# Kernel tuning notes

Hardware: AMD Instinct MI355X
Metric: run time of the kernel (lower is better)

The kernel has to match this reference:

```python
import jax, jax.numpy as jnp
import numpy as np

N_HEADS = 32
N_KV_HEADS = 8
HEAD_DIM = 128
EPS = 1e-6


def _rope_tables(seq_len, dim, base=10000.0):
    inv_freq = 1.0 / (base ** (np.arange(0, dim, 2, dtype=np.float32) / dim))
    t = np.arange(seq_len, dtype=np.float32)
    freqs = np.outer(t, inv_freq)            # [S, d/2]
    emb = np.concatenate([freqs, freqs], -1)  # [S, d]
    return jnp.asarray(np.cos(emb)), jnp.asarray(np.sin(emb))


def setup_inputs() -> dict:
    key = jax.random.key(0)
    ks = jax.random.split(key, 6)
    B, S, H = 1, 2048, 4096
    d = HEAD_DIM
    cos, sin = _rope_tables(S, d)
    return {
        "hidden_states": jax.random.normal(ks[0], (B, S, H), jnp.float32),
        "position_ids": jnp.broadcast_to(jnp.arange(S, dtype=jnp.int64 if jax.config.jax_enable_x64 else jnp.int32), (B, S)),
        "Wq": jax.random.normal(ks[1], (N_HEADS * d, H), jnp.float32) * 0.02,
        "Wk": jax.random.normal(ks[2], (N_KV_HEADS * d, H), jnp.float32) * 0.02,
        "Wv": jax.random.normal(ks[3], (N_KV_HEADS * d, H), jnp.float32) * 0.02,
        "Wo": jax.random.normal(ks[4], (H, N_HEADS * d), jnp.float32) * 0.02,
        "q_norm_w": jnp.ones((d,), jnp.float32),
        "k_norm_w": jnp.ones((d,), jnp.float32),
        "cos": cos,
        "sin": sin,
    }


def _rmsnorm(x, w):
    xf = x.astype(jnp.float32)
    var = jnp.mean(xf * xf, axis=-1, keepdims=True)
    return (w * (xf * jax.lax.rsqrt(var + EPS))).astype(x.dtype)


def _rotate_half(x):
    x1, x2 = jnp.split(x, 2, axis=-1)
    return jnp.concatenate([-x2, x1], axis=-1)


def reference(hidden_states, position_ids, Wq, Wk, Wv, Wo, q_norm_w, k_norm_w, cos, sin):
    B, S, H = hidden_states.shape
    d = HEAD_DIM
    n_rep = N_HEADS // N_KV_HEADS

    # projections -> [B, nH, S, d] / [B, nKV, S, d]
    q = (hidden_states @ Wq.T).reshape(B, S, N_HEADS, d).transpose(0, 2, 1, 3)
    k = (hidden_states @ Wk.T).reshape(B, S, N_KV_HEADS, d).transpose(0, 2, 1, 3)
    v = (hidden_states @ Wv.T).reshape(B, S, N_KV_HEADS, d).transpose(0, 2, 1, 3)

    # per-head QK RMSNorm
    q = _rmsnorm(q, q_norm_w)
    k = _rmsnorm(k, k_norm_w)

    # RoPE: cos/sin gathered by position_ids -> [B, 1, S, d]
    c = cos[position_ids][:, None, :, :]
    s = sin[position_ids][:, None, :, :]
    q = q * c + _rotate_half(q) * s
    k = k * c + _rotate_half(k) * s

    # GQA: repeat kv heads
    k = jnp.repeat(k, n_rep, axis=1)
    v = jnp.repeat(v, n_rep, axis=1)

    # causal SDPA
    scale = 1.0 / jnp.sqrt(jnp.asarray(d, jnp.float32))
    scores = jnp.einsum("bhqd,bhkd->bhqk", q, k) * scale
    causal = jnp.tril(jnp.ones((S, S), bool))
    scores = jnp.where(causal[None, None], scores, jnp.finfo(scores.dtype).min)
    probs = jax.nn.softmax(scores, axis=-1)
    attn = jnp.einsum("bhqk,bhkd->bhqd", probs, v)

    out = attn.transpose(0, 2, 1, 3).reshape(B, S, N_HEADS * d)
    return out @ Wo.T
```

## Files before the change

### kernel.cpp

```cpp
#include <hip/hip_runtime.h>


typedef __attribute__((ext_vector_type(4))) float    f32x4;
typedef __attribute__((ext_vector_type(8))) _Float16 f16x8;
typedef __attribute__((ext_vector_type(4))) _Float16 f16x4;
typedef __attribute__((ext_vector_type(2))) _Float16 f16x2;

#define AS1 __attribute__((address_space(1)))
#define AS3 __attribute__((address_space(3)))

static __device__ __forceinline__ void gld_lds16(const void* g, void* l) {
  __builtin_amdgcn_global_load_lds((AS1 void*)(g), (AS3 void*)(l), 16, 0, 0);
}

static __device__ __forceinline__ void barrier_raw() {
  asm volatile("s_barrier" ::: "memory");
}
#define WAIT_VMCNT(n) asm volatile("s_waitcnt vmcnt(" #n ")" ::: "memory")

__global__ void f32_to_f16(const float* __restrict__ src,
                           _Float16* __restrict__ dst, int n4) {
  int i = blockIdx.x * blockDim.x + threadIdx.x;
  if (i >= n4) return;
  float4 v = ((const float4*)src)[i];
  f16x4 o = {(_Float16)v.x, (_Float16)v.y, (_Float16)v.z, (_Float16)v.w};
  ((f16x4*)dst)[i] = o;
}

__global__ void cvt4(const float* __restrict__ s0, const float* __restrict__ s1,
                     const float* __restrict__ s2, const float* __restrict__ s3,
                     _Float16* __restrict__ d0, _Float16* __restrict__ d1,
                     _Float16* __restrict__ d2, _Float16* __restrict__ d3,
                     int n0, int n1, int n2, int n3) {
  int i = blockIdx.x * blockDim.x + threadIdx.x;
  const float* s;
  _Float16* d;
  int j = i;
  if (j < n0) {
    s = s0; d = d0;
  } else if ((j -= n0) < n1) {
    s = s1; d = d1;
  } else if ((j -= n1) < n2) {
    s = s2; d = d2;
  } else if ((j -= n2) < n3) {
    s = s3; d = d3;
  } else {
    return;
  }
  float4 v = ((const float4*)s)[j];
  f16x4 o = {(_Float16)v.x, (_Float16)v.y, (_Float16)v.z, (_Float16)v.w};
  ((f16x4*)d)[j] = o;
}

template <int BN, typename CT>
__global__ __launch_bounds__(512, 2) void gemm256(
    const _Float16* __restrict__ A, const _Float16* __restrict__ B,
    CT* __restrict__ C, int N, int K) {
  constexpr int NI = BN / 64;
  constexpr int NB = NI / 2;
  __shared__ _Float16 lA[2][256 * 64];
  __shared__ _Float16 lB[2][BN * 64];
  const int tid = threadIdx.x;
  const int lane = tid & 63;
  const int wid = tid >> 6;
  const int quad = lane >> 4, l16 = lane & 15;
  const int wr = wid >> 2, wc = wid & 3;
  const int bid = blockIdx.x;
  const int m0 = (bid & 7) * 256;
  const int n0 = (bid >> 3) * BN;

  const int sr = tid >> 3, sch = tid & 7;
  const int swz = l16 & 7;

  f32x4 acc[8][NI];
#pragma unroll
  for (int i = 0; i < 8; i++)
#pragma unroll
    for (int j = 0; j < NI; j++) acc[i][j] = f32x4{0.f, 0.f, 0.f, 0.f};

  const int nt = K >> 6;

  auto stageA = [&](int bb, int h, int kt) {
#pragma unroll
    for (int u = 0; u < 2; ++u) {
      int rl = u * 64 + sr;
      int r = h * 128 + rl;
      int cg = sch ^ (rl & 7);
      gld_lds16(A + (size_t)(m0 + r) * K + kt * 64 + cg * 8,
                &lA[bb][(size_t)r * 64 + sch * 8]);
    }
  };
  auto stageB = [&](int bb, int h, int kt) {
#pragma unroll
    for (int u = 0; u < 2; ++u) {
      int rl = u * 64 + sr;
      int r = h * 128 + rl;
      int cg = sch ^ (rl & 7);
      gld_lds16(B + (size_t)(n0 + r) * K + kt * 64 + cg * 8,
                &lB[bb][(size_t)r * 64 + sch * 8]);
    }
  };

  auto ldA = [&](f16x8* dst, int qm, int bb) {
#pragma unroll
    for (int mi = 0; mi < 4; ++mi)
#pragma unroll
      for (int kk = 0; kk < 2; ++kk) {
        int row = wr * 128 + (qm * 4 + mi) * 16 + l16;
        int ch = (kk * 4 + quad) ^ swz;
        dst[mi * 2 + kk] = *(const f16x8*)&lA[bb][(size_t)row * 64 + ch * 8];
      }
  };
  auto ldB = [&](f16x8* dst, int qn, int bb) {
#pragma unroll
    for (int ni = 0; ni < NB; ++ni)
#pragma unroll
      for (int kk = 0; kk < 2; ++kk) {
        int row = wc * (BN / 4) + (qn * NB + ni) * 16 + l16;
        int ch = (kk * 4 + quad) ^ swz;
        dst[ni * 2 + kk] = *(const f16x8*)&lB[bb][(size_t)row * 64 + ch * 8];
      }
  };
  auto mmQ = [&](const f16x8* af, const f16x8* bf, int qm, int qn) {
    __builtin_amdgcn_s_setprio(1);
    __builtin_amdgcn_sched_barrier(0);
#pragma unroll
    for (int mi = 0; mi < 4; ++mi)
#pragma unroll
      for (int ni = 0; ni < NB; ++ni)
#pragma unroll
        for (int kk = 0; kk < 2; ++kk)
          acc[qm * 4 + mi][qn * NB + ni] =
              __builtin_amdgcn_mfma_f32_16x16x32_f16(
                  af[mi * 2 + kk], bf[ni * 2 + kk],
                  acc[qm * 4 + mi][qn * NB + ni], 0, 0, 0);
    __builtin_amdgcn_sched_barrier(0);
    __builtin_amdgcn_s_setprio(0);
  };

  stageA(0, 0, 0);
  stageA(0, 1, 0);
  stageB(0, 0, 0);
  if constexpr (BN == 256) stageB(0, 1, 0);
  stageB(1, 0, 1);
  if constexpr (BN == 256) stageB(1, 1, 1);
  if constexpr (BN == 256) {
    WAIT_VMCNT(4);
  } else {
    WAIT_VMCNT(2);
  }
  barrier_raw();

  f16x8 af[8], b0[2 * NB], b1[2 * NB];
  for (int t = 0; t < nt; ++t) {
    const int b = t & 1;
    const int tn1 = (t + 1 < nt) ? t + 1 : t;
    const int tn2 = (t + 2 < nt) ? t + 2 : t;
    ldA(af, 0, b);
    ldB(b0, 0, b);
    stageA(b ^ 1, 0, tn1);
    barrier_raw();
    mmQ(af, b0, 0, 0);
    barrier_raw();
    ldB(b1, 1, b);
    stageA(b ^ 1, 1, tn1);
    barrier_raw();
    mmQ(af, b1, 0, 1);
    barrier_raw();
    ldA(af, 1, b);
    stageB(b, 0, tn2);
    barrier_raw();
    mmQ(af, b1, 1, 1);
    barrier_raw();
    if constexpr (BN == 256) stageB(b, 1, tn2);
    if constexpr (BN == 256) {
      WAIT_VMCNT(4);
    } else {
      WAIT_VMCNT(2);
    }
    barrier_raw();
    mmQ(af, b0, 1, 0);
    barrier_raw();
  }

#pragma unroll
  for (int mi8 = 0; mi8 < 8; ++mi8) {
    int m = m0 + wr * 128 + mi8 * 16 + quad * 4;
#pragma unroll
    for (int ni = 0; ni < NI; ++ni) {
      int n = n0 + wc * (BN / 4) + ni * 16 + l16;
      CT* cp = C + (size_t)m * N + n;
#pragma unroll
      for (int r = 0; r < 4; ++r) cp[(size_t)r * N] = (CT)acc[mi8][ni][r];
    }
  }
}

__global__ void norm_rope(const _Float16* __restrict__ raw, int row_stride,
                          int col_off, const float* __restrict__ w,
                          const float* __restrict__ cosb,
                          const float* __restrict__ sinb,
                          const int* __restrict__ pos,
                          _Float16* __restrict__ out, int nh_log2, int S) {
  int gt = blockIdx.x * blockDim.x + threadIdx.x;
  int wid = gt >> 6, lane = gt & 63;
  int h = wid & ((1 << nh_log2) - 1);
  int s = wid >> nh_log2;
  const _Float16* x = raw + (size_t)s * row_stride + col_off + h * 128;
  f16x2 v2 = *(const f16x2*)&x[lane * 2];
  float vx = (float)v2.x, vy = (float)v2.y;
  float ss = vx * vx + vy * vy;
#pragma unroll
  for (int m = 1; m < 64; m <<= 1) ss += __shfl_xor(ss, m);
  float inv = rsqrtf(ss * (1.f / 128.f) + 1e-6f);
  int p = pos[s];
  float n0 = vx * inv * w[lane * 2];
  float n1 = vy * inv * w[lane * 2 + 1];
  float p0 = __shfl_xor(n0, 32);
  float p1 = __shfl_xor(n1, 32);
  float r0 = (lane < 32) ? -p0 : p0;
  float r1 = (lane < 32) ? -p1 : p1;
  float c0 = cosb[p * 128 + lane * 2], c1 = cosb[p * 128 + lane * 2 + 1];
  float s0 = sinb[p * 128 + lane * 2], s1 = sinb[p * 128 + lane * 2 + 1];
  f16x2 o;
  o.x = (_Float16)(n0 * c0 + r0 * s0);
  o.y = (_Float16)(n1 * c1 + r1 * s1);
  *(f16x2*)&out[((size_t)h * S + s) * 128 + lane * 2] = o;
}

__global__ __launch_bounds__(256) void v_trans(const _Float16* __restrict__ vraw,
                                               int row_stride,
                                               _Float16* __restrict__ vt,
                                               int S) {
  __shared__ _Float16 tile[64][72];
  int s0 = blockIdx.x * 64, c0 = blockIdx.y * 64;
  int t = threadIdx.x;
  int r = t >> 2, cq = (t & 3) * 16;
  const _Float16* src = vraw + (size_t)(s0 + r) * row_stride + c0 + cq;
  f16x8 u0 = *(const f16x8*)&src[0];
  f16x8 u1 = *(const f16x8*)&src[8];
#pragma unroll
  for (int j = 0; j < 8; j++) {
    tile[r][cq + j] = u0[j];
    tile[r][cq + 8 + j] = u1[j];
  }
  __syncthreads();
  int orow = t >> 2, sq = (t & 3) * 16;
  _Float16* dst = vt + (size_t)(c0 + orow) * S + s0 + sq;
  f16x8 a, b;
#pragma unroll
  for (int j = 0; j < 8; j++) a[j] = tile[sq + j][orow];
#pragma unroll
  for (int j = 0; j < 8; j++) b[j] = tile[sq + 8 + j][orow];
  *(f16x8*)&dst[0] = a;
  *(f16x8*)&dst[8] = b;
}

__global__ __launch_bounds__(256, 2) void flash_attn(
    const _Float16* __restrict__ Qh, const _Float16* __restrict__ Kh,
    const _Float16* __restrict__ Vt, _Float16* __restrict__ Oout, int S) {
  __shared__ _Float16 lK[3][32 * 128];
  __shared__ _Float16 lV[3][128 * 32];
  __shared__ _Float16 plds[4][16][40];
  const int wave = threadIdx.x >> 6, lane = threadIdx.x & 63;
  const int quad = lane >> 4, l16 = lane & 15;

  const int flat = blockIdx.y * gridDim.x + blockIdx.x;
  const int head = (flat & 7) * 4 + ((flat >> 3) & 3);
  const int px   = flat >> 5;
  const int kvh  = head >> 2;
  const _Float16* K = Kh + (size_t)kvh * S * 128;
  const _Float16* V = Vt + (size_t)kvh * 128 * S;

  const int ksw = l16 & 7;
  const int vchunk = quad ^ ((l16 >> 1) & 3);
  const float scale = 0.08838834764831845f;
  const float Mc = 5.0f;

  auto stage = [&](int kt, int bi) {
#pragma unroll
    for (int u = 0; u < 2; ++u) {
      int j = wave * 2 + u;
      int rK = j * 4 + (lane >> 4);
      int cK = (lane & 15) ^ (rK & 7);
      gld_lds16(K + (size_t)(kt * 32 + rK) * 128 + cK * 8, &lK[bi][j * 512]);
      int rV = j * 16 + (lane >> 2);
      int cV = (lane & 3) ^ ((rV >> 1) & 3);
      gld_lds16(V + (size_t)rV * S + kt * 32 + cV * 8, &lV[bi][j * 512]);
    }
  };

#pragma unroll
  for (int seg = 0; seg < 2; ++seg) {
    const int tile = seg ? (31 - px) : px;
    const int q0 = tile * 64;
    const int wq = q0 + wave * 16;
    const _Float16* Q = Qh + ((size_t)head * S + wq) * 128;

    f16x8 qf[4];
#pragma unroll
    for (int kq = 0; kq < 4; kq++)
      qf[kq] = *(const f16x8*)&Q[(size_t)l16 * 128 + kq * 32 + quad * 8];

    f32x4 o[8];
#pragma unroll
    for (int t = 0; t < 8; t++) o[t] = f32x4{0.f, 0.f, 0.f, 0.f};
    float l_i = 0.f;
    const int q_row = wq + l16;
    const int ktend = 2 * tile + 1;

    stage(0, 0);
    stage(1, 1);
    WAIT_VMCNT(4);
    barrier_raw();

    for (int kt = 0; kt <= ktend; ++kt) {
      const int cur = kt % 3;
      const bool more = (kt + 2 <= ktend);
      if (more) stage(kt + 2, (kt + 2) % 3);
      if (kt * 32 <= wq + 15) {
        f32x4 sc[2];
        sc[0] = f32x4{0.f, 0.f, 0.f, 0.f};
        sc[1] = f32x4{0.f, 0.f, 0.f, 0.f};
#pragma unroll
        for (int mt = 0; mt < 2; mt++)
#pragma unroll
          for (int kq = 0; kq < 4; kq++) {
            f16x8 kf = *(const f16x8*)&lK[cur][(mt * 16 + l16) * 128 +
                                              (((kq * 4 + quad) ^ ksw) * 8)];
            sc[mt] = __builtin_amdgcn_mfma_f32_16x16x32_f16(kf, qf[kq], sc[mt],
                                                            0, 0, 0);
          }
        float p[2][4];
        float rsum = 0.f;
#pragma unroll
        for (int mt = 0; mt < 2; mt++)
#pragma unroll
          for (int r = 0; r < 4; r++) {
            int kcol = kt * 32 + mt * 16 + quad * 4 + r;
            float e = __expf(fmaf(sc[mt][r], scale, -Mc));
            e = (kcol <= q_row) ? e : 0.f;
            p[mt][r] = e;
            rsum += e;
          }
        rsum += __shfl_xor(rsum, 16);
        rsum += __shfl_xor(rsum, 32);
        l_i += rsum;
        f16x4 pk0 = {(_Float16)p[0][0], (_Float16)p[0][1], (_Float16)p[0][2],
                     (_Float16)p[0][3]};
        f16x4 pk1 = {(_Float16)p[1][0], (_Float16)p[1][1], (_Float16)p[1][2],
                     (_Float16)p[1][3]};
        *(f16x4*)&plds[wave][l16][quad * 4] = pk0;
        *(f16x4*)&plds[wave][l16][16 + quad * 4] = pk1;
        f16x8 pf = *(const f16x8*)&plds[wave][l16][quad * 8];
#pragma unroll
        for (int t = 0; t < 8; t++) {
          f16x8 vf = *(const f16x8*)&lV[cur][(t * 16 + l16) * 32 + vchunk * 8];
          o[t] = __builtin_amdgcn_mfma_f32_16x16x32_f16(vf, pf, o[t], 0, 0, 0);
        }
      }
      if (more) {
        WAIT_VMCNT(4);
      } else {
        WAIT_VMCNT(0);
      }
      barrier_raw();
    }

    const float invl = 1.f / l_i;
    _Float16* op = Oout + (size_t)q_row * 4096 + head * 128 + quad * 4;
#pragma unroll
    for (int t = 0; t < 8; t++) {
      f16x4 ov = {(_Float16)(o[t][0] * invl), (_Float16)(o[t][1] * invl),
                  (_Float16)(o[t][2] * invl), (_Float16)(o[t][3] * invl)};
      *(f16x4*)&op[t * 16] = ov;
    }
  }
}

extern "C" void kernel_launch(void* const* d_in, const int* in_sizes, int n_in,
                              void* d_out, int out_size, void* d_ws,
                              size_t ws_size, hipStream_t stream) {
  const int S = 2048, H = 4096, NH = 32, NKV = 8, D = 128;
  const int NQKV = NH * D + 2 * NKV * D;
  const float* hs   = (const float*)d_in[0];
  const int*   pos  = (const int*)d_in[1];
  const float* Wq   = (const float*)d_in[2];
  const float* Wk   = (const float*)d_in[3];
  const float* Wv   = (const float*)d_in[4];
  const float* Wo   = (const float*)d_in[5];
  const float* qw   = (const float*)d_in[6];
  const float* kw   = (const float*)d_in[7];
  const float* cosb = (const float*)d_in[8];
  const float* sinb = (const float*)d_in[9];
  float* out = (float*)d_out;

  char* ws = (char*)d_ws;
  _Float16* wqkv    = (_Float16*)(ws + 0);
  _Float16* hid_bf  = (_Float16*)(ws + 50331648);
  _Float16* qkv_f16 = (_Float16*)(ws + 67108864);
  _Float16* q_bf    = (_Float16*)(ws + 117440512);
  _Float16* k_bf    = (_Float16*)(ws + 134217728);
  _Float16* v_t     = (_Float16*)(ws + 138412032);
  _Float16* attn_bf = (_Float16*)(ws + 96468992);
  _Float16* wo_bf   = (_Float16*)(ws + 0);

  const int n_hs4 = S * H / 4;
  const int n_wq4 = NH * D * H / 4;
  const int n_wk4 = NKV * D * H / 4;
  const int n_wv4 = NKV * D * H / 4;
  const int ncvt = n_hs4 + n_wq4 + n_wk4 + n_wv4;
  cvt4<<<(ncvt + 255) / 256, 256, 0, stream>>>(
      hs, Wq, Wk, Wv, hid_bf, wqkv, wqkv + (size_t)H * H,
      wqkv + (size_t)(H + NKV * D) * H, n_hs4, n_wq4, n_wk4, n_wv4);

  gemm256<256, _Float16><<<dim3((NQKV / 256) * 8), 512, 0, stream>>>(
      hid_bf, wqkv, qkv_f16, NQKV, H);
  f32_to_f16<<<(H * H / 4 + 255) / 256, 256, 0, stream>>>(Wo, wo_bf, H * H / 4);

  norm_rope<<<S * NH / 4, 256, 0, stream>>>(qkv_f16, NQKV, 0, qw, cosb, sinb,
                                            pos, q_bf, 5, S);
  norm_rope<<<S * NKV / 4, 256, 0, stream>>>(qkv_f16, NQKV, H, kw, cosb, sinb,
                                             pos, k_bf, 3, S);
  v_trans<<<dim3(S / 64, NKV * D / 64), 256, 0, stream>>>(
      qkv_f16 + (size_t)(H + NKV * D), NQKV, v_t, S);

  flash_attn<<<dim3(16, NH), 256, 0, stream>>>(q_bf, k_bf, v_t, attn_bf, S);

  gemm256<128, float><<<dim3((H / 128) * 8), 512, 0, stream>>>(attn_bf, wo_bf,
                                                               out, H, H);
}
```

Measured before the change: 522.5 us.

## Double per-wave query rows in flash attention to reuse K/V fragments

Each wave now processes 32 query rows (two 16-row MFMA tiles) instead of 16, so every K and V fragment read from LDS feeds two MFMAs, and the block covers 128 query rows. The grid is halved to 8x32 blocks and launch bounds relaxed to one block per SIMD occupancy hint, and s_setprio is raised around the MFMA sections. This cuts LDS traffic and K/V staging per query row but raises register pressure, lowers block count (256 blocks) and makes causal load balancing coarser.

```diff
diff --git a/kernel.cpp b/kernel.cpp
--- a/kernel.cpp
+++ b/kernel.cpp
@@ -256,12 +256,12 @@
   *(f16x8*)&dst[8] = b;
 }
 
-__global__ __launch_bounds__(256, 2) void flash_attn(
+__global__ __launch_bounds__(256, 1) void flash_attn(
     const _Float16* __restrict__ Qh, const _Float16* __restrict__ Kh,
     const _Float16* __restrict__ Vt, _Float16* __restrict__ Oout, int S) {
   __shared__ _Float16 lK[3][32 * 128];
   __shared__ _Float16 lV[3][128 * 32];
-  __shared__ _Float16 plds[4][16][40];
+  __shared__ _Float16 plds[4][2][16][40];
   const int wave = threadIdx.x >> 6, lane = threadIdx.x & 63;
   const int quad = lane >> 4, l16 = lane & 15;
 
@@ -292,22 +292,26 @@
 
 #pragma unroll
   for (int seg = 0; seg < 2; ++seg) {
-    const int tile = seg ? (31 - px) : px;
-    const int q0 = tile * 64;
-    const int wq = q0 + wave * 16;
+    const int tile = seg ? (15 - px) : px;
+    const int q0 = tile * 128;
+    const int wq = q0 + wave * 32;
     const _Float16* Q = Qh + ((size_t)head * S + wq) * 128;
 
-    f16x8 qf[4];
-#pragma unroll
-    for (int kq = 0; kq < 4; kq++)
-      qf[kq] = *(const f16x8*)&Q[(size_t)l16 * 128 + kq * 32 + quad * 8];
-
-    f32x4 o[8];
-#pragma unroll
-    for (int t = 0; t < 8; t++) o[t] = f32x4{0.f, 0.f, 0.f, 0.f};
-    float l_i = 0.f;
-    const int q_row = wq + l16;
-    const int ktend = 2 * tile + 1;
+    f16x8 qf[2][4];
+#pragma unroll
+    for (int jq = 0; jq < 2; jq++)
+#pragma unroll
+      for (int kq = 0; kq < 4; kq++)
+        qf[jq][kq] = *(const f16x8*)&Q[(size_t)(jq * 16 + l16) * 128 +
+                                       kq * 32 + quad * 8];
+
+    f32x4 o[8][2];
+#pragma unroll
+    for (int t = 0; t < 8; t++)
+#pragma unroll
+      for (int jq = 0; jq < 2; jq++) o[t][jq] = f32x4{0.f, 0.f, 0.f, 0.f};
+    float l_i[2] = {0.f, 0.f};
+    const int ktend = 4 * tile + 3;
 
     stage(0, 0);
     stage(1, 1);
@@ -318,46 +322,64 @@
       const int cur = kt % 3;
       const bool more = (kt + 2 <= ktend);
       if (more) stage(kt + 2, (kt + 2) % 3);
-      if (kt * 32 <= wq + 15) {
-        f32x4 sc[2];
-        sc[0] = f32x4{0.f, 0.f, 0.f, 0.f};
-        sc[1] = f32x4{0.f, 0.f, 0.f, 0.f};
+      if (kt * 32 <= wq + 31) {
+        f32x4 sc[2][2];
+#pragma unroll
+        for (int mt = 0; mt < 2; mt++)
+#pragma unroll
+          for (int jq = 0; jq < 2; jq++) sc[mt][jq] = f32x4{0.f, 0.f, 0.f, 0.f};
+        __builtin_amdgcn_s_setprio(1);
 #pragma unroll
         for (int mt = 0; mt < 2; mt++)
 #pragma unroll
           for (int kq = 0; kq < 4; kq++) {
             f16x8 kf = *(const f16x8*)&lK[cur][(mt * 16 + l16) * 128 +
                                               (((kq * 4 + quad) ^ ksw) * 8)];
-            sc[mt] = __builtin_amdgcn_mfma_f32_16x16x32_f16(kf, qf[kq], sc[mt],
-                                                            0, 0, 0);
+#pragma unroll
+            for (int jq = 0; jq < 2; jq++)
+              sc[mt][jq] = __builtin_amdgcn_mfma_f32_16x16x32_f16(
+                  kf, qf[jq][kq], sc[mt][jq], 0, 0, 0);
           }
-        float p[2][4];
-        float rsum = 0.f;
-#pragma unroll
-        for (int mt = 0; mt < 2; mt++)
-#pragma unroll
-          for (int r = 0; r < 4; r++) {
-            int kcol = kt * 32 + mt * 16 + quad * 4 + r;
-            float e = __expf(fmaf(sc[mt][r], scale, -Mc));
-            e = (kcol <= q_row) ? e : 0.f;
-            p[mt][r] = e;
-            rsum += e;
-          }
-        rsum += __shfl_xor(rsum, 16);
-        rsum += __shfl_xor(rsum, 32);
-        l_i += rsum;
-        f16x4 pk0 = {(_Float16)p[0][0], (_Float16)p[0][1], (_Float16)p[0][2],
-                     (_Float16)p[0][3]};
-        f16x4 pk1 = {(_Float16)p[1][0], (_Float16)p[1][1], (_Float16)p[1][2],
-                     (_Float16)p[1][3]};
-        *(f16x4*)&plds[wave][l16][quad * 4] = pk0;
-        *(f16x4*)&plds[wave][l16][16 + quad * 4] = pk1;
-        f16x8 pf = *(const f16x8*)&plds[wave][l16][quad * 8];
+        __builtin_amdgcn_s_setprio(0);
+        f16x8 pf[2];
+#pragma unroll
+        for (int jq = 0; jq < 2; jq++) {
+          const int q_row = wq + jq * 16 + l16;
+          float p[2][4];
+          float rsum = 0.f;
+#pragma unroll
+          for (int mt = 0; mt < 2; mt++)
+#pragma unroll
+            for (int r = 0; r < 4; r++) {
+              int kcol = kt * 32 + mt * 16 + quad * 4 + r;
+              float e = __expf(fmaf(sc[mt][jq][r], scale, -Mc));
+              e = (kcol <= q_row) ? e : 0.f;
+              p[mt][r] = e;
+              rsum += e;
+            }
+          rsum += __shfl_xor(rsum, 16);
+          rsum += __shfl_xor(rsum, 32);
+          l_i[jq] += rsum;
+          f16x4 pk0 = {(_Float16)p[0][0], (_Float16)p[0][1], (_Float16)p[0][2],
+                       (_Float16)p[0][3]};
+          f16x4 pk1 = {(_Float16)p[1][0], (_Float16)p[1][1], (_Float16)p[1][2],
+                       (_Float16)p[1][3]};
+          *(f16x4*)&plds[wave][jq][l16][quad * 4] = pk0;
+          *(f16x4*)&plds[wave][jq][l16][16 + quad * 4] = pk1;
+        }
+#pragma unroll
+        for (int jq = 0; jq < 2; jq++)
+          pf[jq] = *(const f16x8*)&plds[wave][jq][l16][quad * 8];
+        __builtin_amdgcn_s_setprio(1);
 #pragma unroll
         for (int t = 0; t < 8; t++) {
           f16x8 vf = *(const f16x8*)&lV[cur][(t * 16 + l16) * 32 + vchunk * 8];
-          o[t] = __builtin_amdgcn_mfma_f32_16x16x32_f16(vf, pf, o[t], 0, 0, 0);
+#pragma unroll
+          for (int jq = 0; jq < 2; jq++)
+            o[t][jq] = __builtin_amdgcn_mfma_f32_16x16x32_f16(vf, pf[jq],
+                                                              o[t][jq], 0, 0, 0);
         }
+        __builtin_amdgcn_s_setprio(0);
       }
       if (more) {
         WAIT_VMCNT(4);
@@ -367,13 +389,17 @@
       barrier_raw();
     }
 
-    const float invl = 1.f / l_i;
-    _Float16* op = Oout + (size_t)q_row * 4096 + head * 128 + quad * 4;
-#pragma unroll
-    for (int t = 0; t < 8; t++) {
-      f16x4 ov = {(_Float16)(o[t][0] * invl), (_Float16)(o[t][1] * invl),
-                  (_Float16)(o[t][2] * invl), (_Float16)(o[t][3] * invl)};
-      *(f16x4*)&op[t * 16] = ov;
+#pragma unroll
+    for (int jq = 0; jq < 2; jq++) {
+      const float invl = 1.f / l_i[jq];
+      const int q_row = wq + jq * 16 + l16;
+      _Float16* op = Oout + (size_t)q_row * 4096 + head * 128 + quad * 4;
+#pragma unroll
+      for (int t = 0; t < 8; t++) {
+        f16x4 ov = {(_Float16)(o[t][jq][0] * invl), (_Float16)(o[t][jq][1] * invl),
+                    (_Float16)(o[t][jq][2] * invl), (_Float16)(o[t][jq][3] * invl)};
+        *(f16x4*)&op[t * 16] = ov;
+      }
     }
   }
 }
@@ -425,7 +451,7 @@
   v_trans<<<dim3(S / 64, NKV * D / 64), 256, 0, stream>>>(
       qkv_f16 + (size_t)(H + NKV * D), NQKV, v_t, S);
 
-  flash_attn<<<dim3(16, NH), 256, 0, stream>>>(q_bf, k_bf, v_t, attn_bf, S);
+  flash_attn<<<dim3(8, NH), 256, 0, stream>>>(q_bf, k_bf, v_t, attn_bf, S);
 
   gemm256<128, float><<<dim3((H / 128) * 8), 512, 0, stream>>>(attn_bf, wo_bf,
                                                                out, H, H);
```

Measured after the change: 553.2 us. 1.06x slower.
